# Kernel optimization log

Hardware: AMD Instinct MI355X
Metric: run time of the kernel (lower is better)

Reference implementation:

```python
import jax, jax.numpy as jnp
import numpy as np

B, N, C = 128, 320, 768
H = 12
T = 64    # template tokens (8x8)
S = 256   # search tokens (16x16)


def setup_inputs() -> dict:
    key = jax.random.key(0)
    k1, k2, k3, k4 = jax.random.split(key, 4)
    return {
        "x1": jax.random.normal(k1, (B, N, C), dtype=jnp.float32),
        "x2": jax.random.normal(k2, (B, N, C), dtype=jnp.float32),
        "qkv_w": jax.random.normal(k3, (3 * C, C), dtype=jnp.float32) * 0.02,
        "proj_w": jax.random.normal(k4, (C, C), dtype=jnp.float32) * 0.02,
        "proj_b": jnp.zeros((C,), dtype=jnp.float32),
    }


def reference(x1, x2, qkv_w, proj_w, proj_b):
    # concat template tokens from x1 with search tokens from x2
    x = jnp.concatenate([x1[:, :T, :], x2[:, T:, :]], axis=1)  # [B, N, C]
    b, n, c = x.shape
    d = c // H
    scale = d ** -0.5

    qkv = (x @ qkv_w.T).reshape(b, n, 3, H, d).transpose(2, 0, 3, 1, 4)  # [3,B,H,N,D]
    q, k, v = qkv[0], qkv[1], qkv[2]

    # template -> template self-attention
    q_mt, k_mt, v_mt = q[:, :, :T], k[:, :, :T], v[:, :, :T]
    attn_mt = jax.nn.softmax(jnp.einsum('bhtd,bhsd->bhts', q_mt, k_mt) * scale, axis=-1)
    x_mt = jnp.einsum('bhts,bhsd->bhtd', attn_mt, v_mt).transpose(0, 2, 1, 3).reshape(b, T, c)

    # search -> all cross+self attention
    q_s = q[:, :, T:]
    attn_s = jax.nn.softmax(jnp.einsum('bhqd,bhkd->bhqk', q_s, k) * scale, axis=-1)
    x_s = jnp.einsum('bhqk,bhkd->bhqd', attn_s, v).transpose(0, 2, 1, 3).reshape(b, S, c)

    out = jnp.concatenate([x_mt, x_s], axis=1) @ proj_w.T + proj_b
    return out
```

## Files before the change

### kernel.cpp

```cpp
#include <hip/hip_runtime.h>
#include <hip/hip_bf16.h>
#include <stdint.h>

#define B_   128
#define N_   320
#define C_   768
#define H_   12
#define D_   64
#define NT_  (B_*N_)
#define K3_  (3*C_)
#define NKT  12
#define TE   (256*64)

typedef __attribute__((ext_vector_type(8))) __bf16 bf16x8;
typedef __attribute__((ext_vector_type(4))) float  f32x4;

__device__ __forceinline__ unsigned short f2bf(float f) {
  union { float f; unsigned u; } v; v.f = f;
  return (unsigned short)((v.u + 0x7fffu + ((v.u >> 16) & 1u)) >> 16);
}

__device__ __forceinline__ void gload16(const unsigned short* g, unsigned short* l) {
  __builtin_amdgcn_global_load_lds((const __attribute__((address_space(1))) void*)g,
                                   (__attribute__((address_space(3))) void*)l,
                                   16, 0, 0);
}

__global__ void prep_x(const float* __restrict__ x1, const float* __restrict__ x2,
                       unsigned short* __restrict__ xb) {
  const unsigned total4 = (unsigned)NT_ * C_ / 4;
  const unsigned stride = gridDim.x * blockDim.x;
  for (unsigned i = blockIdx.x * blockDim.x + threadIdx.x; i < total4; i += stride) {
    unsigned tok = i / (C_ / 4);
    unsigned n   = tok % N_;
    const float* src = (n < 64u) ? x1 : x2;
    float4 v = *(const float4*)(src + (size_t)i * 4u);
    ushort4 o;
    o.x = f2bf(v.x); o.y = f2bf(v.y); o.z = f2bf(v.z); o.w = f2bf(v.w);
    *(ushort4*)(xb + (size_t)i * 4u) = o;
  }
}

__global__ void prep_w(const float* __restrict__ qkv_w, const float* __restrict__ proj_w,
                       unsigned short* __restrict__ wq, unsigned short* __restrict__ wp) {
  const int QKV4 = (K3_ * C_) / 4;
  const int Q4   = (C_ * C_) / 4;
  const int P4   = (C_ * C_) / 4;
  int i = blockIdx.x * 256 + threadIdx.x;
  if (i < QKV4) {
    float s = (i < Q4) ? 0.125f : 1.0f;
    float4 v = *(const float4*)(qkv_w + (size_t)i * 4);
    ushort4 o;
    o.x = f2bf(v.x * s); o.y = f2bf(v.y * s); o.z = f2bf(v.z * s); o.w = f2bf(v.w * s);
    *(ushort4*)(wq + (size_t)i * 4) = o;
  } else if (i < QKV4 + P4) {
    int j = i - QKV4;
    float4 v = *(const float4*)(proj_w + (size_t)j * 4);
    ushort4 o;
    o.x = f2bf(v.x); o.y = f2bf(v.y); o.z = f2bf(v.z); o.w = f2bf(v.w);
    *(ushort4*)(wp + (size_t)j * 4) = o;
  }
}

#define BARR do { asm volatile("" ::: "memory"); __builtin_amdgcn_s_barrier(); asm volatile("" ::: "memory"); } while(0)
#define DSW  asm volatile("s_waitcnt lgkmcnt(0)" ::: "memory")
#define VMW(n) asm volatile("s_waitcnt vmcnt(" #n ")" ::: "memory")
#define NOPW do {} while(0)
#define PRIO1 __builtin_amdgcn_s_setprio(1)
#define PRIO0 __builtin_amdgcn_s_setprio(0)
#define RD(base, off) (*(const bf16x8*)((base) + (off)))

#define LDA_Q(QQ, PARX) do { \
    a_[0][0] = RD(bAk0, (PARX)*32768 + (QQ)*8192);        \
    a_[0][1] = RD(bAk1, (PARX)*32768 + (QQ)*8192);        \
    a_[1][0] = RD(bAk0, (PARX)*32768 + (QQ)*8192 + 2048); \
    a_[1][1] = RD(bAk1, (PARX)*32768 + (QQ)*8192 + 2048); } while(0)

#define LDB(PARX) do { \
    _Pragma("unroll") for (int nf = 0; nf < 4; ++nf) { \
      b_[0][nf] = RD(bBk0, (PARX)*32768 + nf*2048); \
      b_[1][nf] = RD(bBk1, (PARX)*32768 + nf*2048); } } while(0)

#define MFMA_Q(QQ) do { \
    _Pragma("unroll") for (int ks = 0; ks < 2; ++ks) \
    _Pragma("unroll") for (int f = 0; f < 2; ++f) \
    _Pragma("unroll") for (int nf = 0; nf < 4; ++nf) \
      acc[(QQ)*2+f][nf] = __builtin_amdgcn_mfma_f32_16x16x32_bf16(a_[f][ks], b_[ks][nf], acc[(QQ)*2+f][nf], 0, 0, 0); \
  } while(0)

#define STGA_H0(PARX) do { gload16(gA00, dA + ((PARX)^1)*TE);        gload16(gA01, dA + ((PARX)^1)*TE + 512);  gA00 += 64; gA01 += 64; } while(0)
#define STGA_H1(PARX) do { gload16(gA10, dA + ((PARX)^1)*TE + 8192); gload16(gA11, dA + ((PARX)^1)*TE + 8704); gA10 += 64; gA11 += 64; } while(0)
#define STGB_H0(PARX) do { gload16(gB00, dB + (PARX)*TE);            gload16(gB01, dB + (PARX)*TE + 512);      gB00 += 64; gB01 += 64; } while(0)
#define STGB_H1(PARX) do { gload16(gB10, dB + (PARX)*TE + 8192);     gload16(gB11, dB + (PARX)*TE + 8704);     gB10 += 64; gB11 += 64; } while(0)

#define KTILE(PARX, SA_, SB_, W1_, W3_) do { \
    LDA_Q(0, PARX); LDB(PARX); if (SA_) STGA_H0(PARX); \
    BARR; DSW; PRIO1; MFMA_Q(0); PRIO0; BARR; \
    LDA_Q(1, PARX); if (SA_) STGA_H1(PARX); \
    BARR; DSW; PRIO1; MFMA_Q(1); PRIO0; W1_; BARR; \
    LDA_Q(2, PARX); if (SB_) STGB_H0(PARX); \
    BARR; DSW; PRIO1; MFMA_Q(2); PRIO0; BARR; \
    LDA_Q(3, PARX); if (SB_) STGB_H1(PARX); \
    BARR; DSW; PRIO1; MFMA_Q(3); PRIO0; W3_; BARR; \
  } while(0)

__device__ __forceinline__ void kloop256(const unsigned short* __restrict__ Ag,
                                         const unsigned short* __restrict__ Wg,
                                         int row0, int col0,
                                         unsigned short* As, unsigned short* Bs,
                                         f32x4 (&acc)[8][4]) {
  const int tid = threadIdx.x, lane = tid & 63, w = tid >> 6;
  const int wr = w >> 2, wc = w & 3;
  const int lr = lane & 15, kg = lane >> 4;
  const int rr = lane >> 3;
  const int sp = (lane & 7) ^ rr;

  const char* bAk0 = (const char*)As + wr*4096 + lr*128 + (((0*4)+kg) ^ (lr & 7))*16;
  const char* bAk1 = (const char*)As + wr*4096 + lr*128 + (((1*4)+kg) ^ (lr & 7))*16;
  const char* bBk0 = (const char*)Bs + wc*8192 + lr*128 + (((0*4)+kg) ^ (lr & 7))*16;
  const char* bBk1 = (const char*)Bs + wc*8192 + lr*128 + (((1*4)+kg) ^ (lr & 7))*16;

  const unsigned short* gA00 = Ag + (size_t)(row0 +   0 + w*16 + 0 + rr)*768 + 1*64 + sp*8;
  const unsigned short* gA01 = Ag + (size_t)(row0 +   0 + w*16 + 8 + rr)*768 + 1*64 + sp*8;
  const unsigned short* gA10 = Ag + (size_t)(row0 + 128 + w*16 + 0 + rr)*768 + 1*64 + sp*8;
  const unsigned short* gA11 = Ag + (size_t)(row0 + 128 + w*16 + 8 + rr)*768 + 1*64 + sp*8;
  const unsigned short* gB00 = Wg + (size_t)(col0 +   0 + w*16 + 0 + rr)*768 + 2*64 + sp*8;
  const unsigned short* gB01 = Wg + (size_t)(col0 +   0 + w*16 + 8 + rr)*768 + 2*64 + sp*8;
  const unsigned short* gB10 = Wg + (size_t)(col0 + 128 + w*16 + 0 + rr)*768 + 2*64 + sp*8;
  const unsigned short* gB11 = Wg + (size_t)(col0 + 128 + w*16 + 8 + rr)*768 + 2*64 + sp*8;

  unsigned short* dA = As + w*1024;
  unsigned short* dB = Bs + w*1024;

  gload16(gA00 - 64,  dA);              gload16(gA01 - 64,  dA + 512);
  gload16(gA10 - 64,  dA + 8192);       gload16(gA11 - 64,  dA + 8704);
  gload16(gB00 - 128, dB);              gload16(gB01 - 128, dB + 512);
  gload16(gB10 - 128, dB + 8192);       gload16(gB11 - 128, dB + 8704);
  gload16(gB00 - 64,  dB + TE);         gload16(gB01 - 64,  dB + TE + 512);
  gload16(gB10 - 64,  dB + TE + 8192);  gload16(gB11 - 64,  dB + TE + 8704);
  VMW(4);
  BARR;

  bf16x8 a_[2][2], b_[2][4];
#pragma unroll 1
  for (int tt = 0; tt < 5; ++tt) {
    KTILE(0, 1, 1, VMW(8), VMW(6));
    KTILE(1, 1, 1, VMW(8), VMW(6));
  }
  KTILE(0, 1, 0, VMW(8), VMW(2));
  KTILE(1, 0, 0, VMW(0), NOPW);
}

__global__ void __launch_bounds__(512, 2) gemm_qkv(const unsigned short* __restrict__ A,
                                                   const unsigned short* __restrict__ W,
                                                   unsigned short* __restrict__ qb,
                                                   unsigned short* __restrict__ kb,
                                                   unsigned short* __restrict__ vb) {
  __shared__ __align__(16) unsigned short As[2 * TE];
  __shared__ __align__(16) unsigned short Bs[2 * TE];
  const int tid = threadIdx.x, lane = tid & 63, w = tid >> 6;
  const int wr = w >> 2, wc = w & 3;
  const int lr = lane & 15, kg = lane >> 4;
  const int bid = blockIdx.x;
  const int wg = (bid & 7) * 180 + (bid >> 3);
  const int bm = wg / 9, bn = wg % 9;
  const int row0 = bm * 256, col0 = bn * 256;

  f32x4 acc[8][4] = {};
  kloop256(A, W, row0, col0, As, Bs, acc);

  const int which = bn / 3;
  const int colq  = (bn % 3) * 256 + wc * 64;
  if (which == 2) {
#pragma unroll
    for (int mf = 0; mf < 8; ++mf) {
      const int m0 = row0 + (mf >> 1) * 64 + wr * 32 + (mf & 1) * 16 + kg * 4;
      const unsigned bq = (unsigned)m0 / 320u;
      const unsigned t0 = (unsigned)m0 - bq * 320u;
#pragma unroll
      for (int nf = 0; nf < 4; ++nf) {
        const int nn = colq + nf * 16 + lr;
        const int h = nn >> 6, dd = nn & 63;
        ushort4 o;
        o.x = f2bf(acc[mf][nf][0]); o.y = f2bf(acc[mf][nf][1]);
        o.z = f2bf(acc[mf][nf][2]); o.w = f2bf(acc[mf][nf][3]);
        *(ushort4*)&vb[(((int)bq * 12 + h) * 64 + dd) * 320 + (int)t0] = o;
      }
    }
  } else {
    unsigned short* dst = (which == 0) ? qb : kb;
#pragma unroll
    for (int mf = 0; mf < 8; ++mf) {
      const int m0 = row0 + (mf >> 1) * 64 + wr * 32 + (mf & 1) * 16 + kg * 4;
      const unsigned bq = (unsigned)m0 / 320u;
      const unsigned t0 = (unsigned)m0 - bq * 320u;
#pragma unroll
      for (int nf = 0; nf < 4; ++nf) {
        const int nn = colq + nf * 16 + lr;
        const int h = nn >> 6, dd = nn & 63;
        const int base = (((int)bq * 12 + h) * 320 + (int)t0) * 64 + dd;
#pragma unroll
        for (int r = 0; r < 4; r++)
          dst[base + r * 64] = f2bf(acc[mf][nf][r]);
      }
    }
  }
}

__global__ void __launch_bounds__(256) attn(const unsigned short* __restrict__ qb,
                                            const unsigned short* __restrict__ kb,
                                            const unsigned short* __restrict__ vb,
                                            unsigned short* __restrict__ ab) {
  __shared__ __align__(16) unsigned short Ks[64 * 64];
  __shared__ __align__(16) unsigned short Vt[64 * 64];
  __shared__ __align__(16) unsigned short Pl[4 * 16 * 64];
  const int bid = blockIdx.x;
  const int qt = bid % 5, bh = bid / 5;
  const int tid = threadIdx.x, lane = tid & 63, w = tid >> 6;
  const int lr = lane & 15, kg = lane >> 4;

  const int qrow = qt * 64 + w * 16 + lr;
  const unsigned short* qptr = qb + (bh * 320 + qrow) * 64;
  const bf16x8 qa0 = *(const bf16x8*)(qptr + kg * 8);
  const bf16x8 qa1 = *(const bf16x8*)(qptr + 32 + kg * 8);

  f32x4 o[4] = {};
  float mrun[4] = {-1e30f, -1e30f, -1e30f, -1e30f};
  float lrun[4] = {0.f, 0.f, 0.f, 0.f};
  const int nchunk = (qt == 0) ? 1 : 5;

  const int c0 = w, c1 = w + 4;
  const int srow0 = c0 * 8 + (lane >> 3);
  const int srow1 = c1 * 8 + (lane >> 3);
  const int slot  = lane & 7;
  const int part0 = slot ^ (srow0 & 7);
  const int part1 = slot ^ (srow1 & 7);
  const unsigned short* kbase = kb + bh * 320 * 64;
  const unsigned short* vbase = vb + bh * 64 * 320;
  unsigned short* lk0 = &Ks[c0 * 512];
  unsigned short* lk1 = &Ks[c1 * 512];
  unsigned short* lv0 = &Vt[c0 * 512];
  unsigned short* lv1 = &Vt[c1 * 512];
  char* PwB = (char*)&Pl[w * 1024];

  for (int kc = 0; kc < nchunk; kc++) {
    gload16(kbase + (kc * 64 + srow0) * 64 + part0 * 8, lk0);
    gload16(kbase + (kc * 64 + srow1) * 64 + part1 * 8, lk1);
    gload16(vbase + srow0 * 320 + kc * 64 + part0 * 8, lv0);
    gload16(vbase + srow1 * 320 + kc * 64 + part1 * 8, lv1);
    __syncthreads();

    f32x4 s[4];
#pragma unroll
    for (int kt = 0; kt < 4; kt++) {
      const int key = kt * 16 + lr;
      const char* kr = (const char*)Ks + key * 128;
      const unsigned sw = (unsigned)((key & 7) << 4);
      bf16x8 k0 = *(const bf16x8*)(kr + ((kg * 16) ^ sw));
      bf16x8 k1 = *(const bf16x8*)(kr + ((64 + kg * 16) ^ sw));
      f32x4 z = {0.f, 0.f, 0.f, 0.f};
      z = __builtin_amdgcn_mfma_f32_16x16x32_bf16(qa0, k0, z, 0, 0, 0);
      z = __builtin_amdgcn_mfma_f32_16x16x32_bf16(qa1, k1, z, 0, 0, 0);
      s[kt] = z;
    }

#pragma unroll
    for (int r = 0; r < 4; r++) {
      float rm = fmaxf(fmaxf(s[0][r], s[1][r]), fmaxf(s[2][r], s[3][r]));
      rm = fmaxf(rm, __shfl_xor(rm, 1));
      rm = fmaxf(rm, __shfl_xor(rm, 2));
      rm = fmaxf(rm, __shfl_xor(rm, 4));
      rm = fmaxf(rm, __shfl_xor(rm, 8));
      const float mn = fmaxf(mrun[r], rm);
      const float alpha = __expf(mrun[r] - mn);
      mrun[r] = mn;
      const int q = kg * 4 + r;
      char* prow = PwB + q * 128;
      const unsigned sw = (unsigned)((q & 7) << 4);
      float rs = 0.f;
#pragma unroll
      for (int kt = 0; kt < 4; kt++) {
        const float p = __expf(s[kt][r] - mn);
        rs += p;
        const int key = kt * 16 + lr;
        *(unsigned short*)(prow + ((key * 2) ^ sw)) = f2bf(p);
      }
      rs += __shfl_xor(rs, 1);
      rs += __shfl_xor(rs, 2);
      rs += __shfl_xor(rs, 4);
      rs += __shfl_xor(rs, 8);
      lrun[r] = lrun[r] * alpha + rs;
#pragma unroll
      for (int dt = 0; dt < 4; dt++) o[dt][r] *= alpha;
    }

    asm volatile("s_waitcnt lgkmcnt(0)" ::: "memory");

    {
      const char* par = (const char*)PwB + lr * 128;
      const unsigned swp = (unsigned)((lr & 7) << 4);
      bf16x8 p0 = *(const bf16x8*)(par + ((kg * 16) ^ swp));
      bf16x8 p1 = *(const bf16x8*)(par + ((64 + kg * 16) ^ swp));
#pragma unroll
      for (int dt = 0; dt < 4; dt++) {
        const int d = dt * 16 + lr;
        const char* vr = (const char*)Vt + d * 128;
        const unsigned swv = (unsigned)((d & 7) << 4);
        bf16x8 v0 = *(const bf16x8*)(vr + ((kg * 16) ^ swv));
        bf16x8 v1 = *(const bf16x8*)(vr + ((64 + kg * 16) ^ swv));
        o[dt] = __builtin_amdgcn_mfma_f32_16x16x32_bf16(p0, v0, o[dt], 0, 0, 0);
        o[dt] = __builtin_amdgcn_mfma_f32_16x16x32_bf16(p1, v1, o[dt], 0, 0, 0);
      }
    }
    __syncthreads();
  }

  const int b = bh / 12, h = bh - b * 12;
#pragma unroll
  for (int r = 0; r < 4; r++) {
    const float inv = 1.0f / lrun[r];
    const int token = b * 320 + qt * 64 + w * 16 + kg * 4 + r;
    unsigned short* orow = ab + token * 768 + h * 64;
#pragma unroll
    for (int dt = 0; dt < 4; dt++)
      orow[dt * 16 + lr] = f2bf(o[dt][r] * inv);
  }
}

__global__ void __launch_bounds__(512, 2) gemm_proj(const unsigned short* __restrict__ A,
                                                    const unsigned short* __restrict__ W,
                                                    const float* __restrict__ bias,
                                                    float* __restrict__ out) {
  __shared__ __align__(16) unsigned short As[2 * TE];
  __shared__ __align__(16) unsigned short Bs[2 * TE];
  const int tid = threadIdx.x, lane = tid & 63, w = tid >> 6;
  const int wr = w >> 2, wc = w & 3;
  const int lr = lane & 15, kg = lane >> 4;
  const int bid = blockIdx.x;
  const int wg = (bid & 7) * 60 + (bid >> 3);
  const int bm = wg / 3, bn = wg % 3;
  const int row0 = bm * 256, col0 = bn * 256;

  f32x4 acc[8][4] = {};
  kloop256(A, W, row0, col0, As, Bs, acc);

#pragma unroll
  for (int nf = 0; nf < 4; ++nf) {
    const int nn = col0 + wc * 64 + nf * 16 + lr;
    const float bv = bias[nn];
#pragma unroll
    for (int mf = 0; mf < 8; ++mf) {
      const int m0 = row0 + (mf >> 1) * 64 + wr * 32 + (mf & 1) * 16 + kg * 4;
      float* po = out + (size_t)m0 * 768 + nn;
#pragma unroll
      for (int r = 0; r < 4; r++)
        po[(size_t)r * 768] = acc[mf][nf][r] + bv;
    }
  }
}

extern "C" void kernel_launch(void* const* d_in, const int* in_sizes, int n_in,
                              void* d_out, int out_size, void* d_ws, size_t ws_size,
                              hipStream_t stream) {
  (void)in_sizes; (void)n_in; (void)out_size; (void)ws_size;
  const float* x1     = (const float*)d_in[0];
  const float* x2     = (const float*)d_in[1];
  const float* qkv_w  = (const float*)d_in[2];
  const float* proj_w = (const float*)d_in[3];
  const float* proj_b = (const float*)d_in[4];
  float* out = (float*)d_out;

  const size_t TOK = (size_t)NT_ * C_;
  unsigned short* xb = (unsigned short*)d_ws;
  unsigned short* qb = xb + TOK;
  unsigned short* kb = qb + TOK;
  unsigned short* vb = kb + TOK;
  unsigned short* ab = vb + TOK;
  unsigned short* wq = ab + TOK;
  unsigned short* wp = wq + (size_t)K3_ * C_;

  prep_x<<<8192, 256, 0, stream>>>(x1, x2, xb);
  prep_w<<<2304, 256, 0, stream>>>(qkv_w, proj_w, wq, wp);
  gemm_qkv<<<160 * 9, 512, 0, stream>>>(xb, wq, qb, kb, vb);
  attn<<<1536 * 5, 256, 0, stream>>>(qb, kb, vb, ab);
  gemm_proj<<<160 * 3, 512, 0, stream>>>(ab, wp, proj_b, out);
}
```

Before: 420.7 us.

## Make QKV and proj GEMMs persistent with cross-tile prefetch and swapped-operand MFMA stores

Result: no change. 415.6 us (-1.2%).

```diff
diff --git a/kernel.cpp b/kernel.cpp
--- a/kernel.cpp
+++ b/kernel.cpp
@@ -65,7 +65,6 @@
 #define BARR do { asm volatile("" ::: "memory"); __builtin_amdgcn_s_barrier(); asm volatile("" ::: "memory"); } while(0)
 #define DSW  asm volatile("s_waitcnt lgkmcnt(0)" ::: "memory")
 #define VMW(n) asm volatile("s_waitcnt vmcnt(" #n ")" ::: "memory")
-#define NOPW do {} while(0)
 #define PRIO1 __builtin_amdgcn_s_setprio(1)
 #define PRIO0 __builtin_amdgcn_s_setprio(0)
 #define RD(base, off) (*(const bf16x8*)((base) + (off)))
@@ -81,75 +80,85 @@
       b_[0][nf] = RD(bBk0, (PARX)*32768 + nf*2048); \
       b_[1][nf] = RD(bBk1, (PARX)*32768 + nf*2048); } } while(0)
 
-#define MFMA_Q(QQ) do { \
+#define MFN(QQ) do { \
     _Pragma("unroll") for (int ks = 0; ks < 2; ++ks) \
     _Pragma("unroll") for (int f = 0; f < 2; ++f) \
     _Pragma("unroll") for (int nf = 0; nf < 4; ++nf) \
       acc[(QQ)*2+f][nf] = __builtin_amdgcn_mfma_f32_16x16x32_bf16(a_[f][ks], b_[ks][nf], acc[(QQ)*2+f][nf], 0, 0, 0); \
   } while(0)
 
+#define MFS(QQ) do { \
+    _Pragma("unroll") for (int ks = 0; ks < 2; ++ks) \
+    _Pragma("unroll") for (int f = 0; f < 2; ++f) \
+    _Pragma("unroll") for (int nf = 0; nf < 4; ++nf) \
+      acc[(QQ)*2+f][nf] = __builtin_amdgcn_mfma_f32_16x16x32_bf16(b_[ks][nf], a_[f][ks], acc[(QQ)*2+f][nf], 0, 0, 0); \
+  } while(0)
+
 #define STGA_H0(PARX) do { gload16(gA00, dA + ((PARX)^1)*TE);        gload16(gA01, dA + ((PARX)^1)*TE + 512);  gA00 += 64; gA01 += 64; } while(0)
 #define STGA_H1(PARX) do { gload16(gA10, dA + ((PARX)^1)*TE + 8192); gload16(gA11, dA + ((PARX)^1)*TE + 8704); gA10 += 64; gA11 += 64; } while(0)
 #define STGB_H0(PARX) do { gload16(gB00, dB + (PARX)*TE);            gload16(gB01, dB + (PARX)*TE + 512);      gB00 += 64; gB01 += 64; } while(0)
 #define STGB_H1(PARX) do { gload16(gB10, dB + (PARX)*TE + 8192);     gload16(gB11, dB + (PARX)*TE + 8704);     gB10 += 64; gB11 += 64; } while(0)
 
-#define KTILE(PARX, SA_, SB_, W1_, W3_) do { \
-    LDA_Q(0, PARX); LDB(PARX); if (SA_) STGA_H0(PARX); \
-    BARR; DSW; PRIO1; MFMA_Q(0); PRIO0; BARR; \
-    LDA_Q(1, PARX); if (SA_) STGA_H1(PARX); \
-    BARR; DSW; PRIO1; MFMA_Q(1); PRIO0; W1_; BARR; \
-    LDA_Q(2, PARX); if (SB_) STGB_H0(PARX); \
-    BARR; DSW; PRIO1; MFMA_Q(2); PRIO0; BARR; \
-    LDA_Q(3, PARX); if (SB_) STGB_H1(PARX); \
-    BARR; DSW; PRIO1; MFMA_Q(3); PRIO0; W3_; BARR; \
+#define KTILE(MF, PARX, W1_, W3_) do { \
+    LDA_Q(0, PARX); LDB(PARX); STGA_H0(PARX); \
+    BARR; DSW; PRIO1; MF(0); PRIO0; BARR; \
+    LDA_Q(1, PARX); STGA_H1(PARX); \
+    BARR; DSW; PRIO1; MF(1); PRIO0; W1_; BARR; \
+    LDA_Q(2, PARX); STGB_H0(PARX); \
+    BARR; DSW; PRIO1; MF(2); PRIO0; BARR; \
+    LDA_Q(3, PARX); STGB_H1(PARX); \
+    BARR; DSW; PRIO1; MF(3); PRIO0; W3_; BARR; \
   } while(0)
 
-__device__ __forceinline__ void kloop256(const unsigned short* __restrict__ Ag,
-                                         const unsigned short* __restrict__ Wg,
-                                         int row0, int col0,
-                                         unsigned short* As, unsigned short* Bs,
-                                         f32x4 (&acc)[8][4]) {
-  const int tid = threadIdx.x, lane = tid & 63, w = tid >> 6;
-  const int wr = w >> 2, wc = w & 3;
-  const int lr = lane & 15, kg = lane >> 4;
-  const int rr = lane >> 3;
-  const int sp = (lane & 7) ^ rr;
-
-  const char* bAk0 = (const char*)As + wr*4096 + lr*128 + (((0*4)+kg) ^ (lr & 7))*16;
-  const char* bAk1 = (const char*)As + wr*4096 + lr*128 + (((1*4)+kg) ^ (lr & 7))*16;
-  const char* bBk0 = (const char*)Bs + wc*8192 + lr*128 + (((0*4)+kg) ^ (lr & 7))*16;
-  const char* bBk1 = (const char*)Bs + wc*8192 + lr*128 + (((1*4)+kg) ^ (lr & 7))*16;
-
-  const unsigned short* gA00 = Ag + (size_t)(row0 +   0 + w*16 + 0 + rr)*768 + 1*64 + sp*8;
-  const unsigned short* gA01 = Ag + (size_t)(row0 +   0 + w*16 + 8 + rr)*768 + 1*64 + sp*8;
-  const unsigned short* gA10 = Ag + (size_t)(row0 + 128 + w*16 + 0 + rr)*768 + 1*64 + sp*8;
-  const unsigned short* gA11 = Ag + (size_t)(row0 + 128 + w*16 + 8 + rr)*768 + 1*64 + sp*8;
-  const unsigned short* gB00 = Wg + (size_t)(col0 +   0 + w*16 + 0 + rr)*768 + 2*64 + sp*8;
-  const unsigned short* gB01 = Wg + (size_t)(col0 +   0 + w*16 + 8 + rr)*768 + 2*64 + sp*8;
-  const unsigned short* gB10 = Wg + (size_t)(col0 + 128 + w*16 + 0 + rr)*768 + 2*64 + sp*8;
-  const unsigned short* gB11 = Wg + (size_t)(col0 + 128 + w*16 + 8 + rr)*768 + 2*64 + sp*8;
-
-  unsigned short* dA = As + w*1024;
-  unsigned short* dB = Bs + w*1024;
-
-  gload16(gA00 - 64,  dA);              gload16(gA01 - 64,  dA + 512);
-  gload16(gA10 - 64,  dA + 8192);       gload16(gA11 - 64,  dA + 8704);
-  gload16(gB00 - 128, dB);              gload16(gB01 - 128, dB + 512);
-  gload16(gB10 - 128, dB + 8192);       gload16(gB11 - 128, dB + 8704);
-  gload16(gB00 - 64,  dB + TE);         gload16(gB01 - 64,  dB + TE + 512);
-  gload16(gB10 - 64,  dB + TE + 8192);  gload16(gB11 - 64,  dB + TE + 8704);
-  VMW(4);
-  BARR;
-
-  bf16x8 a_[2][2], b_[2][4];
-#pragma unroll 1
-  for (int tt = 0; tt < 5; ++tt) {
-    KTILE(0, 1, 1, VMW(8), VMW(6));
-    KTILE(1, 1, 1, VMW(8), VMW(6));
-  }
-  KTILE(0, 1, 0, VMW(8), VMW(2));
-  KTILE(1, 0, 0, VMW(0), NOPW);
-}
+#define RESETA do { \
+    gA00 = Ag_ + (size_t)row0n*768 + offA00; gA01 = Ag_ + (size_t)row0n*768 + offA01; \
+    gA10 = Ag_ + (size_t)row0n*768 + offA10; gA11 = Ag_ + (size_t)row0n*768 + offA11; } while(0)
+#define RESETB do { \
+    gB00 = Wg_ + (size_t)col0n*768 + offA00; gB01 = Wg_ + (size_t)col0n*768 + offA01; \
+    gB10 = Wg_ + (size_t)col0n*768 + offA10; gB11 = Wg_ + (size_t)col0n*768 + offA11; } while(0)
+
+#define TILE12(MF) do { \
+    _Pragma("unroll 1") for (int tt = 0; tt < 5; ++tt) { \
+      KTILE(MF, 0, VMW(8), VMW(6)); KTILE(MF, 1, VMW(8), VMW(6)); } \
+    RESETB; KTILE(MF, 0, VMW(8), VMW(6)); \
+    RESETA; KTILE(MF, 1, VMW(8), VMW(6)); \
+  } while(0)
+
+#define GEMM_SETUP \
+  const int tid = threadIdx.x, lane = tid & 63, w = tid >> 6; \
+  const int wr = w >> 2, wc = w & 3; \
+  const int lr = lane & 15, kg = lane >> 4; \
+  const int rr = lane >> 3; \
+  const int sp = (lane & 7) ^ rr; \
+  const char* bAk0 = (const char*)As + wr*4096 + lr*128 + ((0*4 + kg) ^ (lr & 7))*16; \
+  const char* bAk1 = (const char*)As + wr*4096 + lr*128 + ((1*4 + kg) ^ (lr & 7))*16; \
+  const char* bBk0 = (const char*)Bs + wc*8192 + lr*128 + ((0*4 + kg) ^ (lr & 7))*16; \
+  const char* bBk1 = (const char*)Bs + wc*8192 + lr*128 + ((1*4 + kg) ^ (lr & 7))*16; \
+  const size_t offA00 = (size_t)(w*16 + rr)*768 + sp*8; \
+  const size_t offA01 = offA00 + (size_t)8*768; \
+  const size_t offA10 = offA00 + (size_t)128*768; \
+  const size_t offA11 = offA01 + (size_t)128*768; \
+  unsigned short* dA = As + w*1024; \
+  unsigned short* dB = Bs + w*1024; \
+  const unsigned short *gA00, *gA01, *gA10, *gA11, *gB00, *gB01, *gB10, *gB11;
+
+#define GEMM_PROLOGUE(row0i, col0i) do { \
+    gA00 = Ag_ + (size_t)(row0i)*768 + offA00 + 64;  gA01 = Ag_ + (size_t)(row0i)*768 + offA01 + 64; \
+    gA10 = Ag_ + (size_t)(row0i)*768 + offA10 + 64;  gA11 = Ag_ + (size_t)(row0i)*768 + offA11 + 64; \
+    gB00 = Wg_ + (size_t)(col0i)*768 + offA00 + 128; gB01 = Wg_ + (size_t)(col0i)*768 + offA01 + 128; \
+    gB10 = Wg_ + (size_t)(col0i)*768 + offA10 + 128; gB11 = Wg_ + (size_t)(col0i)*768 + offA11 + 128; \
+    gload16(gA00 - 64,  dA);              gload16(gA01 - 64,  dA + 512); \
+    gload16(gA10 - 64,  dA + 8192);       gload16(gA11 - 64,  dA + 8704); \
+    gload16(gB00 - 128, dB);              gload16(gB01 - 128, dB + 512); \
+    gload16(gB10 - 128, dB + 8192);       gload16(gB11 - 128, dB + 8704); \
+    gload16(gB00 - 64,  dB + TE);         gload16(gB01 - 64,  dB + TE + 512); \
+    gload16(gB10 - 64,  dB + TE + 8192);  gload16(gB11 - 64,  dB + TE + 8704); \
+    VMW(4); BARR; \
+  } while(0)
+
+#define ACC_ZERO do { \
+    _Pragma("unroll") for (int mf = 0; mf < 8; ++mf) \
+    _Pragma("unroll") for (int nf = 0; nf < 4; ++nf) acc[mf][nf] = vzero; } while(0)
 
 __global__ void __launch_bounds__(512, 2) gemm_qkv(const unsigned short* __restrict__ A,
                                                    const unsigned short* __restrict__ W,
@@ -158,53 +167,74 @@
                                                    unsigned short* __restrict__ vb) {
   __shared__ __align__(16) unsigned short As[2 * TE];
   __shared__ __align__(16) unsigned short Bs[2 * TE];
-  const int tid = threadIdx.x, lane = tid & 63, w = tid >> 6;
-  const int wr = w >> 2, wc = w & 3;
-  const int lr = lane & 15, kg = lane >> 4;
-  const int bid = blockIdx.x;
-  const int wg = (bid & 7) * 180 + (bid >> 3);
-  const int bm = wg / 9, bn = wg % 9;
-  const int row0 = bm * 256, col0 = bn * 256;
-
-  f32x4 acc[8][4] = {};
-  kloop256(A, W, row0, col0, As, Bs, acc);
-
-  const int which = bn / 3;
-  const int colq  = (bn % 3) * 256 + wc * 64;
-  if (which == 2) {
-#pragma unroll
-    for (int mf = 0; mf < 8; ++mf) {
-      const int m0 = row0 + (mf >> 1) * 64 + wr * 32 + (mf & 1) * 16 + kg * 4;
-      const unsigned bq = (unsigned)m0 / 320u;
-      const unsigned t0 = (unsigned)m0 - bq * 320u;
-#pragma unroll
-      for (int nf = 0; nf < 4; ++nf) {
-        const int nn = colq + nf * 16 + lr;
-        const int h = nn >> 6, dd = nn & 63;
-        ushort4 o;
-        o.x = f2bf(acc[mf][nf][0]); o.y = f2bf(acc[mf][nf][1]);
-        o.z = f2bf(acc[mf][nf][2]); o.w = f2bf(acc[mf][nf][3]);
-        *(ushort4*)&vb[(((int)bq * 12 + h) * 64 + dd) * 320 + (int)t0] = o;
+  GEMM_SETUP
+  const unsigned short* Ag_ = A;
+  const unsigned short* Wg_ = W;
+  const int wv = blockIdx.x / 80;
+  const int lb = blockIdx.x - wv * 80;
+
+  const f32x4 vzero = {0.f, 0.f, 0.f, 0.f};
+  f32x4 acc[8][4];
+  ACC_ZERO;
+  bf16x8 a_[2][2], b_[2][4];
+
+  {
+    const int t0i = lb * 6;
+    const int row0i = (t0i / 3) * 256, col0i = (wv * 3 + t0i % 3) * 256;
+    GEMM_PROLOGUE(row0i, col0i);
+  }
+
+  if (wv != 2) {
+    unsigned short* dst = (wv == 0) ? qb : kb;
+#pragma unroll 1
+    for (int j = 0; j < 6; ++j) {
+      const int t = lb * 6 + j, tn = (j < 5) ? t + 1 : t;
+      const int row0c = (t / 3) * 256, cb = (t % 3) * 256;
+      const int row0n = (tn / 3) * 256, col0n = (wv * 3 + tn % 3) * 256;
+      TILE12(MFS);
+#pragma unroll
+      for (int mf = 0; mf < 8; ++mf) {
+        const int tok = row0c + (mf >> 1) * 64 + wr * 32 + (mf & 1) * 16 + lr;
+        const unsigned bq = (unsigned)tok / 320u;
+        const int tt2 = tok - (int)bq * 320;
+#pragma unroll
+        for (int nf = 0; nf < 4; ++nf) {
+          const int nn = cb + wc * 64 + nf * 16 + kg * 4;
+          const int h = nn >> 6, dd = nn & 63;
+          ushort4 o;
+          o.x = f2bf(acc[mf][nf][0]); o.y = f2bf(acc[mf][nf][1]);
+          o.z = f2bf(acc[mf][nf][2]); o.w = f2bf(acc[mf][nf][3]);
+          *(ushort4*)&dst[(size_t)((((int)bq * 12 + h) * 320 + tt2) * 64 + dd)] = o;
+        }
       }
+      ACC_ZERO;
     }
   } else {
-    unsigned short* dst = (which == 0) ? qb : kb;
-#pragma unroll
-    for (int mf = 0; mf < 8; ++mf) {
-      const int m0 = row0 + (mf >> 1) * 64 + wr * 32 + (mf & 1) * 16 + kg * 4;
-      const unsigned bq = (unsigned)m0 / 320u;
-      const unsigned t0 = (unsigned)m0 - bq * 320u;
-#pragma unroll
-      for (int nf = 0; nf < 4; ++nf) {
-        const int nn = colq + nf * 16 + lr;
-        const int h = nn >> 6, dd = nn & 63;
-        const int base = (((int)bq * 12 + h) * 320 + (int)t0) * 64 + dd;
-#pragma unroll
-        for (int r = 0; r < 4; r++)
-          dst[base + r * 64] = f2bf(acc[mf][nf][r]);
+#pragma unroll 1
+    for (int j = 0; j < 6; ++j) {
+      const int t = lb * 6 + j, tn = (j < 5) ? t + 1 : t;
+      const int row0c = (t / 3) * 256, cb = (t % 3) * 256;
+      const int row0n = (tn / 3) * 256, col0n = (wv * 3 + tn % 3) * 256;
+      TILE12(MFN);
+#pragma unroll
+      for (int mf = 0; mf < 8; ++mf) {
+        const int m0 = row0c + (mf >> 1) * 64 + wr * 32 + (mf & 1) * 16 + kg * 4;
+        const unsigned bq = (unsigned)m0 / 320u;
+        const int t0v = m0 - (int)bq * 320;
+#pragma unroll
+        for (int nf = 0; nf < 4; ++nf) {
+          const int nn = cb + wc * 64 + nf * 16 + lr;
+          const int h = nn >> 6, dd = nn & 63;
+          ushort4 o;
+          o.x = f2bf(acc[mf][nf][0]); o.y = f2bf(acc[mf][nf][1]);
+          o.z = f2bf(acc[mf][nf][2]); o.w = f2bf(acc[mf][nf][3]);
+          *(ushort4*)&vb[(size_t)(((((int)bq * 12 + h) * 64 + dd) * 320) + t0v)] = o;
+        }
       }
-    }
-  }
+      ACC_ZERO;
+    }
+  }
+  asm volatile("s_waitcnt vmcnt(0) lgkmcnt(0)" ::: "memory");
 }
 
 __global__ void __launch_bounds__(256) attn(const unsigned short* __restrict__ qb,
@@ -333,30 +363,44 @@
                                                     float* __restrict__ out) {
   __shared__ __align__(16) unsigned short As[2 * TE];
   __shared__ __align__(16) unsigned short Bs[2 * TE];
-  const int tid = threadIdx.x, lane = tid & 63, w = tid >> 6;
-  const int wr = w >> 2, wc = w & 3;
-  const int lr = lane & 15, kg = lane >> 4;
-  const int bid = blockIdx.x;
-  const int wg = (bid & 7) * 60 + (bid >> 3);
-  const int bm = wg / 3, bn = wg % 3;
-  const int row0 = bm * 256, col0 = bn * 256;
-
-  f32x4 acc[8][4] = {};
-  kloop256(A, W, row0, col0, As, Bs, acc);
-
-#pragma unroll
-  for (int nf = 0; nf < 4; ++nf) {
-    const int nn = col0 + wc * 64 + nf * 16 + lr;
-    const float bv = bias[nn];
-#pragma unroll
-    for (int mf = 0; mf < 8; ++mf) {
-      const int m0 = row0 + (mf >> 1) * 64 + wr * 32 + (mf & 1) * 16 + kg * 4;
-      float* po = out + (size_t)m0 * 768 + nn;
-#pragma unroll
-      for (int r = 0; r < 4; r++)
-        po[(size_t)r * 768] = acc[mf][nf][r] + bv;
-    }
-  }
+  GEMM_SETUP
+  const unsigned short* Ag_ = A;
+  const unsigned short* Wg_ = W;
+  const int lb = blockIdx.x;
+
+  const f32x4 vzero = {0.f, 0.f, 0.f, 0.f};
+  f32x4 acc[8][4];
+  ACC_ZERO;
+  bf16x8 a_[2][2], b_[2][4];
+
+  {
+    const int t0i = lb * 2;
+    const int row0i = (t0i / 3) * 256, col0i = (t0i % 3) * 256;
+    GEMM_PROLOGUE(row0i, col0i);
+  }
+
+#pragma unroll 1
+  for (int j = 0; j < 2; ++j) {
+    const int t = lb * 2 + j, tn = (j < 1) ? t + 1 : t;
+    const int row0c = (t / 3) * 256, col0c = (t % 3) * 256;
+    const int row0n = (tn / 3) * 256, col0n = (tn % 3) * 256;
+    TILE12(MFN);
+#pragma unroll
+    for (int nf = 0; nf < 4; ++nf) {
+      const int nn = col0c + wc * 64 + nf * 16 + lr;
+      const float bv = bias[nn];
+#pragma unroll
+      for (int mf = 0; mf < 8; ++mf) {
+        const int m0 = row0c + (mf >> 1) * 64 + wr * 32 + (mf & 1) * 16 + kg * 4;
+        float* po = out + (size_t)m0 * 768 + nn;
+#pragma unroll
+        for (int r = 0; r < 4; r++)
+          po[(size_t)r * 768] = acc[mf][nf][r] + bv;
+      }
+    }
+    ACC_ZERO;
+  }
+  asm volatile("s_waitcnt vmcnt(0) lgkmcnt(0)" ::: "memory");
 }
 
 extern "C" void kernel_launch(void* const* d_in, const int* in_sizes, int n_in,
@@ -381,7 +425,7 @@
 
   prep_x<<<8192, 256, 0, stream>>>(x1, x2, xb);
   prep_w<<<2304, 256, 0, stream>>>(qkv_w, proj_w, wq, wp);
-  gemm_qkv<<<160 * 9, 512, 0, stream>>>(xb, wq, qb, kb, vb);
+  gemm_qkv<<<240, 512, 0, stream>>>(xb, wq, qb, kb, vb);
   attn<<<1536 * 5, 256, 0, stream>>>(qb, kb, vb, ab);
-  gemm_proj<<<160 * 3, 512, 0, stream>>>(ab, wp, proj_b, out);
-}
+  gemm_proj<<<240, 512, 0, stream>>>(ab, wp, proj_b, out);
+}
```
